# Optimization experiments

Measured on AMD Instinct MI355X. Metric: run time of the kernel, lower is better.

## Reference

```python
import jax, jax.numpy as jnp
import numpy as np
from jax import lax

BN_EPS = 1e-5
BNS = 1.0 / np.sqrt(1.0 + BN_EPS)  # eval-mode BatchNorm with mean=0, var=1, gamma=1, beta=0


def setup_inputs() -> dict:
    key = jax.random.key(0)
    ks = jax.random.split(key, 12)
    B, Cin, H, W = 8, 256, 128, 128
    NC, HD, RC, NL = 12, 64, 128, 3
    f = lambda k, shp, s: jax.random.normal(k, shp, jnp.float32) * s
    return dict(
        features=f(ks[0], (B, Cin, H, W), 1.0),
        segmentation=jax.random.uniform(ks[1], (B, NC, H, W), dtype=jnp.float32),
        W_rpn=f(ks[2], (RC, Cin, 3, 3), 0.02), b_rpn=jnp.zeros((RC,), jnp.float32),
        W_node=f(ks[3], (HD, RC), 0.08), b_node=jnp.zeros((HD,), jnp.float32),
        W_e1=f(ks[4], (2 * HD, HD), 0.08), b_e1=jnp.zeros((HD,), jnp.float32),
        W_e2=f(ks[5], (HD, HD), 0.1), b_e2=jnp.zeros((HD,), jnp.float32),
        W_g=f(ks[6], (NL, HD, HD), 0.1), b_g=jnp.zeros((NL, HD), jnp.float32),
        ln_g=jnp.ones((NL, HD), jnp.float32), ln_b=jnp.zeros((NL, HD), jnp.float32),
        glob_emb=f(ks[7], (NC, HD), 0.02),
        W_sp=f(ks[8], (HD, RC), 0.1), b_sp=jnp.zeros((RC,), jnp.float32),
    )


def _forward(features, segmentation, W_rpn, b_rpn, W_node, b_node, W_e1, b_e1,
             W_e2, b_e2, W_g, b_g, ln_g, ln_b, glob_emb, W_sp, b_sp):
    B, NC, H, W = segmentation.shape
    HD = W_node.shape[0]
    NL = W_g.shape[0]

    # ---- RegionProposalNetwork: 3x3 conv + BN(eval) + ReLU ----
    refined = lax.conv_general_dilated(
        features, W_rpn, (1, 1), 'SAME',
        dimension_numbers=('NCHW', 'OIHW', 'NCHW'))
    refined = jax.nn.relu((refined + b_rpn[None, :, None, None]) * BNS)  # [B,RC,H,W]

    # per-class 3x3 maxpool on segmentation, threshold -> binary masks
    pooled = lax.reduce_window(segmentation, -jnp.inf, lax.max,
                               (1, 1, 3, 3), (1, 1, 1, 1), 'SAME')
    masks = (pooled > 0.5).astype(features.dtype)  # [B,NC,H,W]

    # ---- NodeFeatureExtractor (1x1 conv is linear: conv(f*m)=(Wf)*m + b) ----
    yw = jnp.einsum('dk,bkhw->bdhw', W_node, refined)            # [B,HD,H,W]
    z = jax.nn.relu((yw + b_node[None, :, None, None]) * BNS)    # value inside mask region
    masked_sum = jnp.einsum('bdhw,bchw->bcd', z, masks)          # [B,NC,HD]
    mask_sum = masks.sum((2, 3))                                 # [B,NC]
    node_feats = masked_sum / (mask_sum[..., None] + 1e-6)       # [B,NC,HD]

    # ---- EdgeFeatureExtractor: all (i,j), i!=j, gated by class presence ----
    pairs = np.array([(i, j) for i in range(NC) for j in range(NC) if i != j])
    src = jnp.asarray(pairs[:, 0])  # [E]
    dst = jnp.asarray(pairs[:, 1])
    present = (mask_sum > 0).astype(features.dtype)              # [B,NC]
    valid = present[:, src] * present[:, dst]                    # [B,E]
    cat = jnp.concatenate([node_feats[:, src], node_feats[:, dst]], axis=-1)  # [B,E,2HD]
    h = jax.nn.relu(cat @ W_e1 + b_e1)
    edge_attr = (h @ W_e2 + b_e2) * valid[..., None]             # [B,E,HD]

    # ---- TissueGraphNetwork ----
    presence = (node_feats.sum(-1) != 0).astype(features.dtype)[..., None]  # [B,NC,1]
    seg_sum = jax.vmap(lambda m: jax.ops.segment_sum(m, dst, num_segments=NC))
    x = node_feats
    for l in range(NL):
        xw = x @ W_g[l]                                          # [B,NC,HD]
        msgs = xw[:, src] * edge_attr                            # [B,E,HD]
        agg = seg_sum(msgs) + b_g[l]
        xr = jax.nn.relu(agg)
        mu = xr.mean(-1, keepdims=True)
        var = ((xr - mu) ** 2).mean(-1, keepdims=True)
        normed = (xr - mu) / jnp.sqrt(var + 1e-5) * ln_g[l] + ln_b[l]
        x = normed + x if l > 0 else normed
    x = x * presence + glob_emb[None] * (1.0 - presence)         # [B,NC,HD]

    # ---- SpatialProjector ----
    spatial = jnp.einsum('bcd,bchw->bdhw', x, masks)             # [B,HD,H,W]
    out = jnp.einsum('do,bdhw->bohw', W_sp, spatial)             # [B,RC,H,W]
    out = jax.nn.relu((out + b_sp[None, :, None, None]) * BNS)
    return out


def reference(features, segmentation, W_rpn, b_rpn, W_node, b_node, W_e1, b_e1,
              W_e2, b_e2, W_g, b_g, ln_g, ln_b, glob_emb, W_sp, b_sp):
    return _forward(features, segmentation, W_rpn, b_rpn, W_node, b_node,
                    W_e1, b_e1, W_e2, b_e2, W_g, b_g, ln_g, ln_b,
                    glob_emb, W_sp, b_sp)
```

## Files before the change

### kernel.cpp

```cpp
#include <hip/hip_runtime.h>
#include <math.h>

#define BNS_F 0.9999950000374998f

typedef short short8 __attribute__((ext_vector_type(8)));
typedef float f32x4 __attribute__((ext_vector_type(4)));

typedef __attribute__((address_space(3))) void lds_void;
typedef const __attribute__((address_space(1))) void glb_void;

__device__ __forceinline__ unsigned short f2bf(float f) {
    unsigned u = __builtin_bit_cast(unsigned, f);
    unsigned r = (u + 0x7fffu + ((u >> 16) & 1u)) >> 16;
    return (unsigned short)r;
}
__device__ __forceinline__ float bf2f(unsigned short h) {
    unsigned u = ((unsigned)h) << 16;
    return __builtin_bit_cast(float, u);
}

__global__ __launch_bounds__(256) void prep_kernel(
    const float* __restrict__ feat, unsigned short* __restrict__ Fbt,
    const float* __restrict__ Wrpn, unsigned short* __restrict__ Wr,
    const float* __restrict__ seg, float* __restrict__ masks,
    float* __restrict__ mask_sum)
{
    int bid = blockIdx.x;
    int t = threadIdx.x;

    if (bid < 16384) {
        int pxc = bid & 63;
        int icg = (bid >> 6) & 31;
        int b   = bid >> 11;
        int px  = pxc * 256 + t;
        const float* src = feat + ((size_t)(b * 256 + icg * 8)) * 16384 + px;
        unsigned v[4];
        #pragma unroll
        for (int i = 0; i < 4; ++i) {
            unsigned lo = f2bf(src[(size_t)(2 * i)     * 16384]);
            unsigned hi = f2bf(src[(size_t)(2 * i + 1) * 16384]);
            v[i] = lo | (hi << 16);
        }
        uint4 o; o.x = v[0]; o.y = v[1]; o.z = v[2]; o.w = v[3];
        *(uint4*)(Fbt + (((size_t)(b * 32 + icg) * 16384) + px) * 8) = o;
    } else if (bid < 16512) {
        int oc = bid - 16384;
        const float* src = Wrpn + ((size_t)oc * 256 + t) * 9;
        #pragma unroll
        for (int tap = 0; tap < 9; ++tap)
            Wr[((size_t)tap * 128 + oc) * 256 + t] = f2bf(src[tap]);
    } else {
        int mb = bid - 16512;
        int h = (mb & 63) * 2 + (t >> 7);
        int c = (mb >> 6) % 12;
        int b = mb / (64 * 12);
        int px = t & 127;

        const float* s = seg + ((size_t)(b * 12 + c) * 128) * 128;
        float m = -INFINITY;
        #pragma unroll
        for (int dy = -1; dy <= 1; ++dy) {
            int y = h + dy;
            if (y < 0 || y > 127) continue;
            #pragma unroll
            for (int dx = -1; dx <= 1; ++dx) {
                int x = px + dx;
                if (x < 0 || x > 127) continue;
                m = fmaxf(m, s[y * 128 + x]);
            }
        }
        float v = (m > 0.5f) ? 1.0f : 0.0f;
        masks[((size_t)(b * 12 + c) * 128 + h) * 128 + px] = v;

        float cnt = v;
        #pragma unroll
        for (int off = 1; off < 64; off <<= 1) cnt += __shfl_xor(cnt, off, 64);
        if ((t & 63) == 0) atomicAdd(&mask_sum[b * 12 + c], cnt);
    }
}

#define BUF_B 12672
#define CHUNK_STEP (4u * 16384u * 8u)

__global__ __launch_bounds__(512, 8) void conv_node_kernel(
    const unsigned short* __restrict__ Fbt, const unsigned short* __restrict__ Wr,
    const float* __restrict__ brpn, const float* __restrict__ Wnode,
    const float* __restrict__ bnode, const float* __restrict__ masks,
    const float* __restrict__ zero16, float* __restrict__ ms_rep)
{
    __shared__ __align__(16) unsigned char lds[25344];

    int wg = blockIdx.x;
    int bid = (wg & 7) * 256 + (wg >> 3);
    int b    = bid >> 8;
    int h    = (bid >> 1) & 127;
    int px0  = (bid & 1) * 64;

    int t = threadIdx.x;
    int lane = t & 63;
    int wv = __builtin_amdgcn_readfirstlane(t >> 6);
    int kg = lane >> 4;
    int ln15 = lane & 15;

    f32x4 acc[4];
    #pragma unroll
    for (int nt = 0; nt < 4; ++nt) acc[nt] = (f32x4){0.f, 0.f, 0.f, 0.f};

    const unsigned short* zp = (const unsigned short*)zero16;

    const unsigned short* pp0;
    const unsigned short* pp1;
    #pragma unroll
    for (int r = 0; r < 2; ++r) {
        int c = r * 512 + t;
        bool act = (c < 792);
        int row = c / 264;
        int rem = c - row * 264;
        int slot = rem / 66;
        int col = rem - slot * 66;
        int y = h - 1 + row, x = px0 + col - 1;
        bool in = act && ((unsigned)y < 128u) && ((unsigned)x < 128u);
        const unsigned short* p =
            in ? (Fbt + (((size_t)(b * 32 + slot) * 16384) + y * 128 + x) * 8) : zp;
        if (r == 0) pp0 = p; else pp1 = p;
    }

    auto stage = [&](int bsel) {
        unsigned lo0 = (unsigned)bsel * BUF_B + (unsigned)(wv * 64) * 16;
        __builtin_amdgcn_global_load_lds((glb_void*)pp0,
            (lds_void*)(lds + lo0), 16, 0, 0);
        pp0 += (pp0 == zp) ? 0u : CHUNK_STEP;
        if (512 + t < 792) {
            unsigned lo1 = (unsigned)bsel * BUF_B + (unsigned)(512 + wv * 64) * 16;
            __builtin_amdgcn_global_load_lds((glb_void*)pp1,
                (lds_void*)(lds + lo1), 16, 0, 0);
        }
        pp1 += (pp1 == zp) ? 0u : CHUNK_STEP;
    };

    unsigned vb = (unsigned)(kg * 66 + ln15) * 16;
    unsigned laneA = (unsigned)(ln15 * 256 + kg * 8);

    stage(0);
    __syncthreads();

    for (int s = 0; s < 8; ++s) {
        const unsigned short* wpu = Wr + (size_t)(wv * 16) * 256 + s * 32 + laneA;
        unsigned bb = (unsigned)(s & 1) * BUF_B + vb;

        #pragma unroll
        for (int dy = 0; dy < 3; ++dy) {
            #pragma unroll
            for (int dxi = 0; dxi < 3; ++dxi) {
                int tap = dy * 3 + dxi;
                short8 a = *(const short8*)(wpu + (size_t)tap * 32768);
                #pragma unroll
                for (int nt = 0; nt < 4; ++nt) {
                    short8 bf = *(const short8*)
                        (lds + bb + (unsigned)((dy * 264 + dxi) * 16 + nt * 256));
                    acc[nt] = __builtin_amdgcn_mfma_f32_16x16x32_bf16(
                        a, bf, acc[nt], 0, 0, 0);
                }
            }
        }

        if (s < 7) stage((s + 1) & 1);
        __syncthreads();
    }

    unsigned short* refined = (unsigned short*)lds;
    #pragma unroll
    for (int nt = 0; nt < 4; ++nt) {
        #pragma unroll
        for (int r = 0; r < 4; ++r) {
            int oc = wv * 16 + kg * 4 + r;
            int px = nt * 16 + ln15;
            float v = fmaxf((acc[nt][r] + brpn[oc]) * BNS_F, 0.f);
            refined[oc * 66 + px] = f2bf(v);
        }
    }
    __syncthreads();

    float z[8];
    #pragma unroll
    for (int j = 0; j < 8; ++j) z[j] = 0.f;
    const float* wn = Wnode + (size_t)(wv * 8) * 128;
    for (int k = 0; k < 128; ++k) {
        float rv = bf2f(refined[k * 66 + lane]);
        #pragma unroll
        for (int j = 0; j < 8; ++j)
            z[j] = fmaf(wn[j * 128 + k], rv, z[j]);
    }
    #pragma unroll
    for (int j = 0; j < 8; ++j)
        z[j] = fmaxf((z[j] + bnode[wv * 8 + j]) * BNS_F, 0.f);

    int rep = bid & 7;
    const float* mrow = masks + ((size_t)b * 12 * 128 + h) * 128 + px0;
    float* msb = ms_rep + ((size_t)(rep * 8 + b) * 12) * 64 + wv * 8;
    for (int c = 0; c < 12; ++c) {
        float m = mrow[(size_t)c * 16384 + lane];
        #pragma unroll
        for (int j = 0; j < 8; ++j) {
            float v = z[j] * m;
            #pragma unroll
            for (int off2 = 1; off2 < 64; off2 <<= 1) v += __shfl_xor(v, off2, 64);
            if (lane == j) atomicAdd(&msb[c * 64 + j], v);
        }
    }
}

__global__ __launch_bounds__(256) void edge_kernel(
    const float* __restrict__ ms_rep, const float* __restrict__ mask_sum,
    const float* __restrict__ We1, const float* __restrict__ be1,
    const float* __restrict__ We2, const float* __restrict__ be2,
    float* __restrict__ ea_g)
{
    int gb = blockIdx.x;
    int b = gb / 33, eg = gb % 33;
    int wv = threadIdx.x >> 6, d = threadIdx.x & 63;
    int e = eg * 4 + wv;
    int src = e / 11, jj = e % 11;
    int dst = jj + (jj >= src ? 1 : 0);

    float mssrc = 0.f, msdst = 0.f;
    #pragma unroll
    for (int rep = 0; rep < 8; ++rep) {
        mssrc += ms_rep[((size_t)(rep * 8 + b) * 12 + src) * 64 + d];
        msdst += ms_rep[((size_t)(rep * 8 + b) * 12 + dst) * 64 + d];
    }
    float cs = mask_sum[b * 12 + src], cd = mask_sum[b * 12 + dst];
    float nsrc = mssrc / (cs + 1e-6f);
    float ndst = msdst / (cd + 1e-6f);

    float hv = be1[d];
    for (int k = 0; k < 64; ++k) hv = fmaf(__shfl(nsrc, k, 64), We1[k * 64 + d], hv);
    for (int k = 0; k < 64; ++k) hv = fmaf(__shfl(ndst, k, 64), We1[(64 + k) * 64 + d], hv);
    hv = fmaxf(hv, 0.f);
    float av = be2[d];
    for (int k = 0; k < 64; ++k) av = fmaf(__shfl(hv, k, 64), We2[k * 64 + d], av);

    float valid = ((cs > 0.f) ? 1.f : 0.f) * ((cd > 0.f) ? 1.f : 0.f);
    ea_g[((size_t)b * 132 + e) * 64 + d] = av * valid;
}

__global__ __launch_bounds__(256) void graph_kernel(
    const float* __restrict__ ms_rep, const float* __restrict__ mask_sum,
    const float* __restrict__ ea_g,
    const float* __restrict__ Wg, const float* __restrict__ bg,
    const float* __restrict__ lng, const float* __restrict__ lnb,
    const float* __restrict__ glob, const float* __restrict__ Wsp,
    float* __restrict__ xs_out)
{
    __shared__ float nf[12 * 64];
    __shared__ float x [12 * 64];
    __shared__ float xw[12 * 64];
    __shared__ float ea[132 * 64];
    __shared__ float presence[12];

    int b = blockIdx.x;
    int t = threadIdx.x;

    for (int i = t; i < 768; i += 256) {
        int c = i >> 6, d = i & 63;
        float ms = 0.f;
        #pragma unroll
        for (int rep = 0; rep < 8; ++rep)
            ms += ms_rep[((size_t)(rep * 8 + b) * 12 + c) * 64 + d];
        nf[i] = ms / (mask_sum[b * 12 + c] + 1e-6f);
    }
    for (int i = t; i < 132 * 64; i += 256) ea[i] = ea_g[(size_t)b * 8448 + i];
    __syncthreads();

    for (int i = t; i < 768; i += 256) {
        int c = i >> 6;
        float v = nf[i];
        #pragma unroll
        for (int off = 1; off < 64; off <<= 1) v += __shfl_xor(v, off, 64);
        if ((i & 63) == 0) presence[c] = (v != 0.f) ? 1.f : 0.f;
        x[i] = nf[i];
    }
    __syncthreads();

    for (int l = 0; l < 3; ++l) {
        const float* wg = Wg + l * 4096;
        for (int i = t; i < 768; i += 256) {
            int c = i >> 6, d = i & 63;
            float v = 0.f;
            for (int k = 0; k < 64; ++k) v = fmaf(x[c * 64 + k], wg[k * 64 + d], v);
            xw[i] = v;
        }
        __syncthreads();
        for (int i = t; i < 768; i += 256) {
            int j = i >> 6, d = i & 63;
            float agg = bg[l * 64 + d];
            #pragma unroll
            for (int src2 = 0; src2 < 12; ++src2) {
                if (src2 == j) continue;
                int jj2 = j - (j > src2 ? 1 : 0);
                int e = src2 * 11 + jj2;
                agg = fmaf(xw[src2 * 64 + d], ea[e * 64 + d], agg);
            }
            float xr = fmaxf(agg, 0.f);
            float s = xr;
            #pragma unroll
            for (int off = 1; off < 64; off <<= 1) s += __shfl_xor(s, off, 64);
            float mu = s * (1.f / 64.f);
            float df = xr - mu;
            float s2 = df * df;
            #pragma unroll
            for (int off = 1; off < 64; off <<= 1) s2 += __shfl_xor(s2, off, 64);
            float var = s2 * (1.f / 64.f);
            float normed = df * (1.0f / sqrtf(var + 1e-5f)) * lng[l * 64 + d]
                           + lnb[l * 64 + d];
            nf[i] = (l > 0) ? (normed + x[i]) : normed;
        }
        __syncthreads();
        for (int i = t; i < 768; i += 256) x[i] = nf[i];
        __syncthreads();
    }

    for (int i = t; i < 768; i += 256) {
        int c = i >> 6;
        float p = presence[c];
        x[i] = x[i] * p + glob[c * 64 + (i & 63)] * (1.f - p);
    }
    __syncthreads();

    for (int i = t; i < 12 * 128; i += 256) {
        int c = i >> 7, o = i & 127;
        float v = 0.f;
        for (int k = 0; k < 64; ++k) v = fmaf(x[c * 64 + k], Wsp[k * 128 + o], v);
        xs_out[b * 1536 + i] = v;
    }
}

__global__ __launch_bounds__(256) void out_kernel(
    const float* __restrict__ xs, const float* __restrict__ masks,
    const float* __restrict__ bsp, float* __restrict__ out)
{
    __shared__ float xsl[12 * 128];
    __shared__ float ml[12 * 128];
    int bid = blockIdx.x;
    int h = bid & 127;
    int b = bid >> 7;
    int t = threadIdx.x;

    for (int i = t; i < 1536; i += 256) xsl[i] = xs[b * 1536 + i];
    for (int i = t; i < 1536; i += 256) {
        int c = i >> 7, px = i & 127;
        ml[i] = masks[((size_t)(b * 12 + c) * 128 + h) * 128 + px];
    }
    __syncthreads();

    int px = t & 127;
    int og = t >> 7;
    float m[12];
    #pragma unroll
    for (int c = 0; c < 12; ++c) m[c] = ml[c * 128 + px];

    float* ob = out + ((size_t)b * 128 * 128 + h) * 128 + px;
    for (int i = 0; i < 64; ++i) {
        int o = og * 64 + i;
        float s = 0.f;
        #pragma unroll
        for (int c = 0; c < 12; ++c) s = fmaf(xsl[c * 128 + o], m[c], s);
        ob[(size_t)o * 16384] = fmaxf((s + bsp[o]) * BNS_F, 0.f);
    }
}

extern "C" void kernel_launch(void* const* d_in, const int* in_sizes, int n_in,
                              void* d_out, int out_size, void* d_ws, size_t ws_size,
                              hipStream_t stream)
{
    const float* feat  = (const float*)d_in[0];
    const float* seg   = (const float*)d_in[1];
    const float* Wrpn  = (const float*)d_in[2];
    const float* brpn  = (const float*)d_in[3];
    const float* Wnode = (const float*)d_in[4];
    const float* bnode = (const float*)d_in[5];
    const float* We1   = (const float*)d_in[6];
    const float* be1   = (const float*)d_in[7];
    const float* We2   = (const float*)d_in[8];
    const float* be2   = (const float*)d_in[9];
    const float* Wg    = (const float*)d_in[10];
    const float* bg    = (const float*)d_in[11];
    const float* lng   = (const float*)d_in[12];
    const float* lnb   = (const float*)d_in[13];
    const float* glob  = (const float*)d_in[14];
    const float* Wsp   = (const float*)d_in[15];
    const float* bsp   = (const float*)d_in[16];
    float* out = (float*)d_out;

    unsigned short* Fbt = (unsigned short*)d_out;

    float* masks    = (float*)d_ws;
    float* ms_rep   = masks + 1572864;
    float* mask_sum = ms_rep + 49152;
    float* zero16   = mask_sum + 96;
    float* xs       = zero16 + 8;
    float* ea_g     = xs + 12288;
    unsigned short* Wr = (unsigned short*)(ea_g + 67584);

    hipMemsetAsync(ms_rep, 0, (49152 + 96 + 8) * sizeof(float), stream);

    prep_kernel<<<22656, 256, 0, stream>>>(feat, Fbt, Wrpn, Wr, seg, masks, mask_sum);
    conv_node_kernel<<<2048, 512, 0, stream>>>(Fbt, Wr, brpn, Wnode, bnode,
                                               masks, zero16, ms_rep);
    edge_kernel<<<264, 256, 0, stream>>>(ms_rep, mask_sum, We1, be1, We2, be2, ea_g);
    graph_kernel<<<8, 256, 0, stream>>>(ms_rep, mask_sum, ea_g,
                                        Wg, bg, lng, lnb, glob, Wsp, xs);
    out_kernel<<<1024, 256, 0, stream>>>(xs, masks, bsp, out);
}
```

Measured before the change: 468.9 us.

## Widen conv tile to full row with swizzled LDS and vectorize output kernel

The conv+node kernel now gives each 1024-thread workgroup a full 128-pixel row instead of half a row. The halo overhead per row drops and each block's staged input is reused across two N-groups of waves. The LDS layout gets an XOR-style slot swizzle to cut bank conflicts, and the B fragments are loaded ahead of the MFMAs. The output kernel is rewritten to use float4 mask loads and stores, with each thread handling 4 pixels for 16 channels, giving wider memory transactions at the cost of more registers.

After: 491.1 us. 1.05x slower.

```diff
diff --git a/kernel.cpp b/kernel.cpp
--- a/kernel.cpp
+++ b/kernel.cpp
@@ -79,26 +79,27 @@
     }
 }
 
-#define BUF_B 12672
+#define SWZ(col) (((col) >> 1) & 3)
+#define BUF_BYTES 24960
 #define CHUNK_STEP (4u * 16384u * 8u)
 
-__global__ __launch_bounds__(512, 8) void conv_node_kernel(
+__global__ __launch_bounds__(1024, 8) void conv_node_kernel(
     const unsigned short* __restrict__ Fbt, const unsigned short* __restrict__ Wr,
     const float* __restrict__ brpn, const float* __restrict__ Wnode,
     const float* __restrict__ bnode, const float* __restrict__ masks,
     const float* __restrict__ zero16, float* __restrict__ ms_rep)
 {
-    __shared__ __align__(16) unsigned char lds[25344];
+    __shared__ __align__(16) unsigned char lds[49920];
 
     int wg = blockIdx.x;
-    int bid = (wg & 7) * 256 + (wg >> 3);
-    int b    = bid >> 8;
-    int h    = (bid >> 1) & 127;
-    int px0  = (bid & 1) * 64;
+    int bid = (wg & 7) * 128 + (wg >> 3);
+    int h = bid & 127, b = bid >> 7;
 
     int t = threadIdx.x;
     int lane = t & 63;
     int wv = __builtin_amdgcn_readfirstlane(t >> 6);
+    int mg = wv >> 1;
+    int ng = wv & 1;
     int kg = lane >> 4;
     int ln15 = lane & 15;
 
@@ -112,55 +113,59 @@
     const unsigned short* pp1;
     #pragma unroll
     for (int r = 0; r < 2; ++r) {
-        int c = r * 512 + t;
-        bool act = (c < 792);
-        int row = c / 264;
-        int rem = c - row * 264;
-        int slot = rem / 66;
-        int col = rem - slot * 66;
-        int y = h - 1 + row, x = px0 + col - 1;
+        int c = r * 1024 + t;
+        bool act = (c < 1560);
+        int sp = c & 3, cr = c >> 2;
+        int col = cr % 130, row = cr / 130;
+        int sl = (sp - SWZ(col)) & 3;
+        int y = h - 1 + row, x = col - 1;
         bool in = act && ((unsigned)y < 128u) && ((unsigned)x < 128u);
         const unsigned short* p =
-            in ? (Fbt + (((size_t)(b * 32 + slot) * 16384) + y * 128 + x) * 8) : zp;
+            in ? (Fbt + (((size_t)(b * 32 + sl) * 16384) + y * 128 + x) * 8) : zp;
         if (r == 0) pp0 = p; else pp1 = p;
     }
 
     auto stage = [&](int bsel) {
-        unsigned lo0 = (unsigned)bsel * BUF_B + (unsigned)(wv * 64) * 16;
+        unsigned lo0 = (unsigned)bsel * BUF_BYTES + (unsigned)(wv * 64) * 16;
         __builtin_amdgcn_global_load_lds((glb_void*)pp0,
             (lds_void*)(lds + lo0), 16, 0, 0);
         pp0 += (pp0 == zp) ? 0u : CHUNK_STEP;
-        if (512 + t < 792) {
-            unsigned lo1 = (unsigned)bsel * BUF_B + (unsigned)(512 + wv * 64) * 16;
+        if (t < 536) {
+            unsigned lo1 = (unsigned)bsel * BUF_BYTES
+                         + (unsigned)(1024 + wv * 64) * 16;
             __builtin_amdgcn_global_load_lds((glb_void*)pp1,
                 (lds_void*)(lds + lo1), 16, 0, 0);
         }
         pp1 += (pp1 == zp) ? 0u : CHUNK_STEP;
     };
 
-    unsigned vb = (unsigned)(kg * 66 + ln15) * 16;
-    unsigned laneA = (unsigned)(ln15 * 256 + kg * 8);
+    const unsigned short* wA = Wr + (size_t)(mg * 16 + ln15) * 256 + kg * 8;
 
     stage(0);
     __syncthreads();
 
     for (int s = 0; s < 8; ++s) {
-        const unsigned short* wpu = Wr + (size_t)(wv * 16) * 256 + s * 32 + laneA;
-        unsigned bb = (unsigned)(s & 1) * BUF_B + vb;
+        int ic0 = s * 32;
+        const unsigned char* buf = lds + (s & 1) * BUF_BYTES;
 
         #pragma unroll
         for (int dy = 0; dy < 3; ++dy) {
             #pragma unroll
             for (int dxi = 0; dxi < 3; ++dxi) {
                 int tap = dy * 3 + dxi;
-                short8 a = *(const short8*)(wpu + (size_t)tap * 32768);
+                short8 a = *(const short8*)(wA + (size_t)tap * 32768 + ic0);
+                short8 bf[4];
                 #pragma unroll
                 for (int nt = 0; nt < 4; ++nt) {
-                    short8 bf = *(const short8*)
-                        (lds + bb + (unsigned)((dy * 264 + dxi) * 16 + nt * 256));
+                    int col = ng * 64 + nt * 16 + ln15 + dxi;
+                    unsigned off =
+                        (unsigned)((dy * 130 + col) * 4 + ((kg + SWZ(col)) & 3)) * 16;
+                    bf[nt] = *(const short8*)(buf + off);
+                }
+                #pragma unroll
+                for (int nt = 0; nt < 4; ++nt)
                     acc[nt] = __builtin_amdgcn_mfma_f32_16x16x32_bf16(
-                        a, bf, acc[nt], 0, 0, 0);
-                }
+                        a, bf[nt], acc[nt], 0, 0, 0);
             }
         }
 
@@ -171,12 +176,12 @@
     unsigned short* refined = (unsigned short*)lds;
     #pragma unroll
     for (int nt = 0; nt < 4; ++nt) {
+        int px = ng * 64 + nt * 16 + ln15;
         #pragma unroll
         for (int r = 0; r < 4; ++r) {
-            int oc = wv * 16 + kg * 4 + r;
-            int px = nt * 16 + ln15;
+            int oc = mg * 16 + kg * 4 + r;
             float v = fmaxf((acc[nt][r] + brpn[oc]) * BNS_F, 0.f);
-            refined[oc * 66 + px] = f2bf(v);
+            refined[oc * 130 + px] = f2bf(v);
         }
     }
     __syncthreads();
@@ -184,20 +189,20 @@
     float z[8];
     #pragma unroll
     for (int j = 0; j < 8; ++j) z[j] = 0.f;
-    const float* wn = Wnode + (size_t)(wv * 8) * 128;
+    const float* wn = Wnode + (size_t)(mg * 8) * 128;
     for (int k = 0; k < 128; ++k) {
-        float rv = bf2f(refined[k * 66 + lane]);
+        float rv = bf2f(refined[k * 130 + ng * 64 + lane]);
         #pragma unroll
         for (int j = 0; j < 8; ++j)
             z[j] = fmaf(wn[j * 128 + k], rv, z[j]);
     }
     #pragma unroll
     for (int j = 0; j < 8; ++j)
-        z[j] = fmaxf((z[j] + bnode[wv * 8 + j]) * BNS_F, 0.f);
+        z[j] = fmaxf((z[j] + bnode[mg * 8 + j]) * BNS_F, 0.f);
 
     int rep = bid & 7;
-    const float* mrow = masks + ((size_t)b * 12 * 128 + h) * 128 + px0;
-    float* msb = ms_rep + ((size_t)(rep * 8 + b) * 12) * 64 + wv * 8;
+    const float* mrow = masks + ((size_t)b * 12 * 128 + h) * 128 + ng * 64;
+    float* msb = ms_rep + ((size_t)(rep * 8 + b) * 12) * 64 + mg * 8;
     for (int c = 0; c < 12; ++c) {
         float m = mrow[(size_t)c * 16384 + lane];
         #pragma unroll
@@ -340,32 +345,44 @@
     const float* __restrict__ bsp, float* __restrict__ out)
 {
     __shared__ float xsl[12 * 128];
-    __shared__ float ml[12 * 128];
+    __shared__ float4 ml4[12 * 32];
     int bid = blockIdx.x;
     int h = bid & 127;
     int b = bid >> 7;
     int t = threadIdx.x;
 
     for (int i = t; i < 1536; i += 256) xsl[i] = xs[b * 1536 + i];
-    for (int i = t; i < 1536; i += 256) {
-        int c = i >> 7, px = i & 127;
-        ml[i] = masks[((size_t)(b * 12 + c) * 128 + h) * 128 + px];
-    }
-    __syncthreads();
-
-    int px = t & 127;
-    int og = t >> 7;
-    float m[12];
-    #pragma unroll
-    for (int c = 0; c < 12; ++c) m[c] = ml[c * 128 + px];
-
-    float* ob = out + ((size_t)b * 128 * 128 + h) * 128 + px;
-    for (int i = 0; i < 64; ++i) {
-        int o = og * 64 + i;
-        float s = 0.f;
-        #pragma unroll
-        for (int c = 0; c < 12; ++c) s = fmaf(xsl[c * 128 + o], m[c], s);
-        ob[(size_t)o * 16384] = fmaxf((s + bsp[o]) * BNS_F, 0.f);
+    for (int i = t; i < 384; i += 256) {
+        int c = i >> 5, q = i & 31;
+        ml4[i] = ((const float4*)(masks + ((size_t)(b * 12 + c) * 128 + h) * 128))[q];
+    }
+    __syncthreads();
+
+    int q  = t & 31;
+    int o0 = (t >> 5) * 16;
+    float4 m4[12];
+    #pragma unroll
+    for (int c = 0; c < 12; ++c) m4[c] = ml4[c * 32 + q];
+
+    float* ob = out + ((size_t)b * 128) * 16384 + h * 128 + q * 4;
+    #pragma unroll 4
+    for (int i = 0; i < 16; ++i) {
+        int o = o0 + i;
+        float4 s = {0.f, 0.f, 0.f, 0.f};
+        #pragma unroll
+        for (int c = 0; c < 12; ++c) {
+            float w = xsl[c * 128 + o];
+            s.x = fmaf(w, m4[c].x, s.x);
+            s.y = fmaf(w, m4[c].y, s.y);
+            s.z = fmaf(w, m4[c].z, s.z);
+            s.w = fmaf(w, m4[c].w, s.w);
+        }
+        float bb = bsp[o];
+        s.x = fmaxf((s.x + bb) * BNS_F, 0.f);
+        s.y = fmaxf((s.y + bb) * BNS_F, 0.f);
+        s.z = fmaxf((s.z + bb) * BNS_F, 0.f);
+        s.w = fmaxf((s.w + bb) * BNS_F, 0.f);
+        *(float4*)(ob + (size_t)o * 16384) = s;
     }
 }
 
@@ -405,8 +422,8 @@
     hipMemsetAsync(ms_rep, 0, (49152 + 96 + 8) * sizeof(float), stream);
 
     prep_kernel<<<22656, 256, 0, stream>>>(feat, Fbt, Wrpn, Wr, seg, masks, mask_sum);
-    conv_node_kernel<<<2048, 512, 0, stream>>>(Fbt, Wr, brpn, Wnode, bnode,
-                                               masks, zero16, ms_rep);
+    conv_node_kernel<<<1024, 1024, 0, stream>>>(Fbt, Wr, brpn, Wnode, bnode,
+                                                masks, zero16, ms_rep);
     edge_kernel<<<264, 256, 0, stream>>>(ms_rep, mask_sum, We1, be1, We2, be2, ea_g);
     graph_kernel<<<8, 256, 0, stream>>>(ms_rep, mask_sum, ea_g,
                                         Wg, bg, lng, lnb, glob, Wsp, xs);
```
